# Kernel tuning notes

Hardware: AMD Instinct MI355X
Metric: run time of the kernel (lower is better)

## Reference

```python
import jax, jax.numpy as jnp
import numpy as np

N = 100000   # nodes
E = 800000   # directed edges (before self-loops)
D = 64       # hidden_dim
NUM_ROUNDS = 4
EPS = 1e-5


def setup_inputs() -> dict:
    key = jax.random.key(0)
    k0, k1, k2 = jax.random.split(key, 3)
    x = jax.random.normal(k0, (N, D), dtype=jnp.float32)
    edge_index = jax.random.randint(k1, (2, E), 0, N, dtype=jnp.int32)
    W = jax.random.normal(k2, (D, D), dtype=jnp.float32) * (1.0 / np.sqrt(D))
    b = jnp.zeros((D,), dtype=jnp.float32)
    gamma = jnp.ones((D,), dtype=jnp.float32)
    beta = jnp.zeros((D,), dtype=jnp.float32)
    return {"x": x, "edge_index": edge_index, "W": W, "b": b,
            "gamma": gamma, "beta": beta, "num_rounds": NUM_ROUNDS}


def reference(x, edge_index, W, b, gamma, beta, num_rounds):
    n = x.shape[0]
    # GCNConv: add self-loops, symmetric degree normalization D^-1/2 (A+I) D^-1/2
    loops = jnp.arange(n, dtype=edge_index.dtype)
    src = jnp.concatenate([edge_index[0], loops])  # [E+N] message sources
    dst = jnp.concatenate([edge_index[1], loops])  # [E+N] message targets
    deg = jax.ops.segment_sum(jnp.ones_like(dst, dtype=x.dtype), dst, num_segments=n)
    dis = jnp.where(deg > 0, jax.lax.rsqrt(deg), 0.0)  # deg^-1/2, 0 for isolated
    norm = dis[src] * dis[dst]                          # [E+N] edge weights

    for _ in range(num_rounds):
        h = x @ W                                                      # [N, D]
        msgs = h[src] * norm[:, None]                                  # gather [E+N, D]
        agg = jax.ops.segment_sum(msgs, dst, num_segments=n) + b      # scatter-add
        # LayerNorm over feature dim
        mu = agg.mean(axis=-1, keepdims=True)
        var = agg.var(axis=-1, keepdims=True)
        x = (agg - mu) * jax.lax.rsqrt(var + EPS) * gamma + beta
    return x
```

## Files before the change

### kernel.cpp

```cpp
#include <hip/hip_runtime.h>

#define D 64
#define EPSV 1e-5f
#define SLOTP 16
#define SLOTS2 24
#define BSH 9
#define BNODES (1 << BSH)
#define BCAP 8192
#define SRCBITS 17

typedef _Float16 f16;
typedef _Float16 f16x8 __attribute__((ext_vector_type(8)));
typedef float f32x4 __attribute__((ext_vector_type(4)));


__global__ void k_init(int* gcnt, int nbk, const float* __restrict__ W,
                       f16* __restrict__ Wp) {
    const int t = threadIdx.x;
    if (t < nbk) gcnt[t] = 0;
    for (int idx = t; idx < 512; idx += 256) {
        int s = idx >> 8, rem = idx & 255, tt = rem >> 6, l = rem & 63;
        int q = l >> 4, c = l & 15;
#pragma unroll
        for (int j = 0; j < 8; ++j) {
            int k = 32 * s + 8 * q + j;
            Wp[(size_t)idx * 8 + j] = (f16)W[k * D + 16 * tt + c];
        }
    }
}

__global__ __launch_bounds__(256) void k_binA(
    const int* __restrict__ src, const int* __restrict__ dst,
    int* __restrict__ gcnt, unsigned* __restrict__ breg, int e, int nbk) {
    __shared__ int bcnt[256];
    __shared__ int gbase[256];
    const int tid = threadIdx.x;
    if (tid < nbk) bcnt[tid] = 0;
    __syncthreads();

    const int per = (e + gridDim.x - 1) / gridDim.x;
    const int lo = blockIdx.x * per;
    const int hi = min(e, lo + per);

    for (int i = lo + tid; i < hi; i += 256)
        atomicAdd(&bcnt[dst[i] >> BSH], 1);
    __syncthreads();

    if (tid < nbk) {
        int c = bcnt[tid];
        gbase[tid] = (c > 0) ? atomicAdd(&gcnt[tid], c) : 0;
        bcnt[tid] = 0;
    }
    __syncthreads();

    for (int i = lo + tid; i < hi; i += 256) {
        int d_ = dst[i], s_ = src[i];
        int bkt = d_ >> BSH;
        int p = gbase[bkt] + atomicAdd(&bcnt[bkt], 1);
        if (p < BCAP)
            breg[(size_t)bkt * BCAP + p] =
                ((unsigned)(d_ & (BNODES - 1)) << SRCBITS) | (unsigned)s_;
    }
}

__global__ __launch_bounds__(256) void k_binB(
    const int* __restrict__ gcnt, const unsigned* __restrict__ breg,
    unsigned* __restrict__ slots, unsigned* __restrict__ slots2,
    int* __restrict__ cursor, float* __restrict__ disv, int n) {
    __shared__ int scnt[BNODES];
    __shared__ unsigned sbuf[BNODES][SLOTP];
    const int tid = threadIdx.x;
    const int bkt = blockIdx.x;
    const int base = bkt << BSH;
    const int nloc = min(BNODES, n - base);

    for (int i = tid; i < BNODES; i += 256) scnt[i] = 0;
    __syncthreads();

    const int cnt = min(gcnt[bkt], BCAP);
    const unsigned* reg = breg + (size_t)bkt * BCAP;
    for (int i = tid; i < cnt; i += 256) {
        unsigned v = reg[i];
        int ld = v >> SRCBITS;
        unsigned s = v & ((1u << SRCBITS) - 1);
        int p = atomicAdd(&scnt[ld], 1);
        if (p < SLOTP) sbuf[ld][p] = s;
        else if (p < SLOTP + SLOTS2)
            slots2[(size_t)(base + ld) * SLOTS2 + (p - SLOTP)] = s;
    }
    __syncthreads();

    for (int i = tid; i < nloc * 4; i += 256) {
        int ld = i >> 2, part = i & 3;
        ((uint4*)(slots + (size_t)(base + ld) * SLOTP))[part] =
            ((const uint4*)sbuf[ld])[part];
    }
    for (int i = tid; i < nloc; i += 256) {
        int c = scnt[i];
        cursor[base + i] = c;
        disv[base + i] = rsqrtf((float)(c + 1));
    }
}

__global__ __launch_bounds__(256) void k_xform(
    const float* __restrict__ x, const f16* __restrict__ Wp,
    const float* __restrict__ disv, f16* __restrict__ h, int n, int ntiles) {
    const int tile = blockIdx.x * 4 + (threadIdx.x >> 6);
    if (tile >= ntiles) return;
    const int lane = threadIdx.x & 63;
    const int q = lane >> 4, c = lane & 15;

    const f16x8* wp = (const f16x8*)Wp;
    f16x8 w0 = wp[0 * 64 + lane], w1 = wp[1 * 64 + lane];
    f16x8 w2 = wp[2 * 64 + lane], w3 = wp[3 * 64 + lane];
    f16x8 w4 = wp[4 * 64 + lane], w5 = wp[5 * 64 + lane];
    f16x8 w6 = wp[6 * 64 + lane], w7 = wp[7 * 64 + lane];

    const int row0 = tile * 16;
    const int rA = (row0 + c < n) ? (row0 + c) : (n - 1);

    const float4* xr = (const float4*)(x + (size_t)rA * D);
    float4 u0 = xr[2 * q], u1 = xr[2 * q + 1];
    float4 u2 = xr[8 + 2 * q], u3 = xr[9 + 2 * q];
    f16x8 a0 = (f16x8){(f16)u0.x, (f16)u0.y, (f16)u0.z, (f16)u0.w,
                       (f16)u1.x, (f16)u1.y, (f16)u1.z, (f16)u1.w};
    f16x8 a1 = (f16x8){(f16)u2.x, (f16)u2.y, (f16)u2.z, (f16)u2.w,
                       (f16)u3.x, (f16)u3.y, (f16)u3.z, (f16)u3.w};

    f32x4 d0 = {0,0,0,0}, d1 = {0,0,0,0}, d2 = {0,0,0,0}, d3 = {0,0,0,0};
    d0 = __builtin_amdgcn_mfma_f32_16x16x32_f16(a0, w0, d0, 0, 0, 0);
    d1 = __builtin_amdgcn_mfma_f32_16x16x32_f16(a0, w1, d1, 0, 0, 0);
    d2 = __builtin_amdgcn_mfma_f32_16x16x32_f16(a0, w2, d2, 0, 0, 0);
    d3 = __builtin_amdgcn_mfma_f32_16x16x32_f16(a0, w3, d3, 0, 0, 0);
    d0 = __builtin_amdgcn_mfma_f32_16x16x32_f16(a1, w4, d0, 0, 0, 0);
    d1 = __builtin_amdgcn_mfma_f32_16x16x32_f16(a1, w5, d1, 0, 0, 0);
    d2 = __builtin_amdgcn_mfma_f32_16x16x32_f16(a1, w6, d2, 0, 0, 0);
    d3 = __builtin_amdgcn_mfma_f32_16x16x32_f16(a1, w7, d3, 0, 0, 0);

    f32x4 dvv = *(const f32x4*)(disv + row0 + 4 * q);
#pragma unroll
    for (int r = 0; r < 4; ++r) {
        int row = row0 + q * 4 + r;
        if (row < n) {
            f16* hr = h + (size_t)row * D + c;
            hr[0]  = (f16)(d0[r] * dvv[r]);
            hr[16] = (f16)(d1[r] * dvv[r]);
            hr[32] = (f16)(d2[r] * dvv[r]);
            hr[48] = (f16)(d3[r] * dvv[r]);
        }
    }
}

template<bool LAST>
__global__ __launch_bounds__(256) void k_fuse(
    const f16* __restrict__ h, const unsigned* __restrict__ slots,
    const unsigned* __restrict__ slots2, const int* __restrict__ cursor,
    const float* __restrict__ disv,
    const float* __restrict__ bb, const float* __restrict__ gamma,
    const float* __restrict__ beta, const f16* __restrict__ Wp,
    float* __restrict__ out, f16* __restrict__ hnext, int n,
    int sq, int sr) {
    __shared__ __align__(16) f16 ylds[32][72];

    const int xb = blockIdx.x & 7, kb = blockIdx.x >> 3;
    const int bid = (xb < sr ? xb * (sq + 1) : sr * (sq + 1) + (xb - sr) * sq) + kb;

    const int tid = threadIdx.x;
    const int grp = tid >> 3;
    const int fl  = tid & 7;
    const int w = bid * 32 + grp;
    const bool act = (w < n);

    if (act) {
        const int jb = w * SLOTP;
        const int dg = cursor[w];
        const int dgp = (dg < SLOTP) ? dg : SLOTP;

        float acc[8];
        {
            f16x8 sv = *(const f16x8*)(h + (size_t)w * D + fl * 8);
#pragma unroll
            for (int f = 0; f < 8; ++f) acc[f] = (float)sv[f];
        }

        uint4 s0 = *(const uint4*)(slots + jb);
        uint4 s1 = *(const uint4*)(slots + jb + 4);
        uint4 s2 = *(const uint4*)(slots + jb + 8);
        const unsigned idx[12] = {s0.x, s0.y, s0.z, s0.w,
                                  s1.x, s1.y, s1.z, s1.w,
                                  s2.x, s2.y, s2.z, s2.w};
        f16x8 v[12];
#pragma unroll
        for (int k = 0; k < 12; ++k) {
            unsigned u = (k < dg) ? idx[k] : 0u;
            v[k] = *(const f16x8*)(h + (size_t)u * D + fl * 8);
        }
#pragma unroll
        for (int k = 0; k < 12; ++k) {
            float m = (k < dg) ? 1.0f : 0.0f;
#pragma unroll
            for (int f = 0; f < 8; ++f) acc[f] += m * (float)v[k][f];
        }
        if (dgp > 12) {
            uint4 sr4 = *(const uint4*)(slots + jb + 12);
            const unsigned uu[4] = {sr4.x, sr4.y, sr4.z, sr4.w};
#pragma unroll
            for (int k = 0; k < 4; ++k) {
                unsigned u = (12 + k < dgp) ? uu[k] : 0u;
                float m = (12 + k < dgp) ? 1.0f : 0.0f;
                f16x8 vv = *(const f16x8*)(h + (size_t)u * D + fl * 8);
#pragma unroll
                for (int f = 0; f < 8; ++f) acc[f] += m * (float)vv[f];
            }
        }
        if (dg > SLOTP) {
            const unsigned* r2 = slots2 + (size_t)w * SLOTS2;
            int dg2 = dg - SLOTP; if (dg2 > SLOTS2) dg2 = SLOTS2;
#pragma unroll
            for (int base = 0; base < SLOTS2; base += 4) {
                if (base < dg2) {
                    uint4 sr4 = *(const uint4*)(r2 + base);
                    const unsigned uu[4] = {sr4.x, sr4.y, sr4.z, sr4.w};
#pragma unroll
                    for (int k = 0; k < 4; ++k) {
                        unsigned u = (base + k < dg2) ? uu[k] : 0u;
                        float m = (base + k < dg2) ? 1.0f : 0.0f;
                        f16x8 vv = *(const f16x8*)(h + (size_t)u * D + fl * 8);
#pragma unroll
                        for (int f = 0; f < 8; ++f) acc[f] += m * (float)vv[f];
                    }
                }
            }
        }

        const float dv = disv[w];
        const float4 b0 = ((const float4*)bb)[fl * 2],    b1 = ((const float4*)bb)[fl * 2 + 1];
        const float4 g0 = ((const float4*)gamma)[fl * 2], g1 = ((const float4*)gamma)[fl * 2 + 1];
        const float4 e0 = ((const float4*)beta)[fl * 2],  e1 = ((const float4*)beta)[fl * 2 + 1];
        const float bs[8] = {b0.x, b0.y, b0.z, b0.w, b1.x, b1.y, b1.z, b1.w};
        const float gs[8] = {g0.x, g0.y, g0.z, g0.w, g1.x, g1.y, g1.z, g1.w};
        const float es[8] = {e0.x, e0.y, e0.z, e0.w, e1.x, e1.y, e1.z, e1.w};

#pragma unroll
        for (int f = 0; f < 8; ++f) acc[f] = acc[f] * dv + bs[f];

        float s = 0.0f;
#pragma unroll
        for (int f = 0; f < 8; ++f) s += acc[f];
#pragma unroll
        for (int m = 1; m < 8; m <<= 1) s += __shfl_xor(s, m);
        float mu = s * (1.0f / 64.0f);
        float dd[8], qv = 0.0f;
#pragma unroll
        for (int f = 0; f < 8; ++f) { dd[f] = acc[f] - mu; qv += dd[f] * dd[f]; }
#pragma unroll
        for (int m = 1; m < 8; m <<= 1) qv += __shfl_xor(qv, m);
        float rstd = rsqrtf(qv * (1.0f / 64.0f) + EPSV);

        if (LAST) {
            float4 o0, o1;
            o0.x = dd[0] * rstd * gs[0] + es[0]; o0.y = dd[1] * rstd * gs[1] + es[1];
            o0.z = dd[2] * rstd * gs[2] + es[2]; o0.w = dd[3] * rstd * gs[3] + es[3];
            o1.x = dd[4] * rstd * gs[4] + es[4]; o1.y = dd[5] * rstd * gs[5] + es[5];
            o1.z = dd[6] * rstd * gs[6] + es[6]; o1.w = dd[7] * rstd * gs[7] + es[7];
            float4* orow = (float4*)(out + (size_t)w * D);
            orow[fl * 2] = o0; orow[fl * 2 + 1] = o1;
        } else {
            f16x8 yv;
#pragma unroll
            for (int f = 0; f < 8; ++f) yv[f] = (f16)(dd[f] * rstd * gs[f] + es[f]);
            *(f16x8*)(&ylds[grp][fl * 8]) = yv;
        }
    }
    if (LAST) return;

    __syncthreads();

    const int wv = tid >> 6;
    const int lane = tid & 63;
    const int q = lane >> 4, c = lane & 15;

    const f16x8* wp = (const f16x8*)Wp;
    f16x8 wlo = wp[wv * 64 + lane];
    f16x8 whi = wp[(4 + wv) * 64 + lane];

    const int row0 = bid * 32;
#pragma unroll
    for (int rt = 0; rt < 2; ++rt) {
        f16x8 a0 = *(const f16x8*)(&ylds[rt * 16 + c][q * 8]);
        f16x8 a1 = *(const f16x8*)(&ylds[rt * 16 + c][32 + q * 8]);
        f32x4 d = {0, 0, 0, 0};
        d = __builtin_amdgcn_mfma_f32_16x16x32_f16(a0, wlo, d, 0, 0, 0);
        d = __builtin_amdgcn_mfma_f32_16x16x32_f16(a1, whi, d, 0, 0, 0);

        const int rbase = row0 + rt * 16;
        f32x4 dvv = *(const f32x4*)(disv + rbase + 4 * q);
#pragma unroll
        for (int r = 0; r < 4; ++r) {
            int row = rbase + q * 4 + r;
            if (row < n)
                hnext[(size_t)row * D + wv * 16 + c] = (f16)(d[r] * dvv[r]);
        }
    }
}


extern "C" void kernel_launch(void* const* d_in, const int* in_sizes, int n_in,
                              void* d_out, int out_size, void* d_ws, size_t ws_size,
                              hipStream_t stream) {
    const float* x0    = (const float*)d_in[0];
    const int*   ei    = (const int*)d_in[1];
    const float* W     = (const float*)d_in[2];
    const float* b     = (const float*)d_in[3];
    const float* gamma = (const float*)d_in[4];
    const float* beta  = (const float*)d_in[5];

    const int N = in_sizes[0] / D;
    const int E = in_sizes[1] / 2;
    const int* src = ei;
    const int* dst = ei + E;
    const int nbk = (N + BNODES - 1) >> BSH;

    char* ws = (char*)d_ws;
    size_t off = 0;
    auto alloc = [&](size_t bytes) {
        off = (off + 255) & ~(size_t)255;
        void* p = ws + off;
        off += bytes;
        return p;
    };
    int*      cursor = (int*)alloc((size_t)N * 4);
    unsigned* slots  = (unsigned*)alloc((size_t)N * SLOTP * 4);
    unsigned* slots2 = (unsigned*)alloc((size_t)N * SLOTS2 * 4);
    int*      gcnt   = (int*)alloc((size_t)nbk * 4);
    unsigned* breg   = (unsigned*)alloc((size_t)nbk * BCAP * 4);
    float*    disv   = (float*)alloc((size_t)(N + 32) * 4);
    f16*      Wp     = (f16*)alloc(512 * 8 * 2);
    f16*      hA     = (f16*)alloc((size_t)N * D * 2);
    f16*      hB     = (f16*)alloc((size_t)N * D * 2);
    (void)ws_size;

    k_init<<<1, 256, 0, stream>>>(gcnt, nbk, W, Wp);
    k_binA<<<128, 256, 0, stream>>>(src, dst, gcnt, breg, E, nbk);
    k_binB<<<nbk, 256, 0, stream>>>(gcnt, breg, slots, slots2, cursor, disv, N);

    float* out = (float*)d_out;
    const int ntiles = (N + 15) / 16;
    const int GX = (ntiles + 3) / 4;
    const int GG = (N + 31) / 32;
    const int sq = GG / 8, sr = GG % 8;

    k_xform<<<GX, 256, 0, stream>>>(x0, Wp, disv, hA, N, ntiles);
    k_fuse<false><<<GG, 256, 0, stream>>>(hA, slots, slots2, cursor, disv, b, gamma,
                                          beta, Wp, nullptr, hB, N, sq, sr);
    k_fuse<false><<<GG, 256, 0, stream>>>(hB, slots, slots2, cursor, disv, b, gamma,
                                          beta, Wp, nullptr, hA, N, sq, sr);
    k_fuse<false><<<GG, 256, 0, stream>>>(hA, slots, slots2, cursor, disv, b, gamma,
                                          beta, Wp, nullptr, hB, N, sq, sr);
    k_fuse<true><<<GG, 256, 0, stream>>>(hB, slots, slots2, cursor, disv, b, gamma,
                                         beta, Wp, out, nullptr, N, sq, sr);
}
```

Measured before the change: 215.2 us.

## Fuse input transform into binning kernel and pack degree into slot word

```diff
diff --git a/kernel.cpp b/kernel.cpp
--- a/kernel.cpp
+++ b/kernel.cpp
@@ -8,6 +8,8 @@
 #define BNODES (1 << BSH)
 #define BCAP 8192
 #define SRCBITS 17
+#define SRCMASK ((1u << SRCBITS) - 1)
+#define DGSHIFT 26
 
 typedef _Float16 f16;
 typedef _Float16 f16x8 __attribute__((ext_vector_type(8)));
@@ -66,7 +68,8 @@
 __global__ __launch_bounds__(256) void k_binB(
     const int* __restrict__ gcnt, const unsigned* __restrict__ breg,
     unsigned* __restrict__ slots, unsigned* __restrict__ slots2,
-    int* __restrict__ cursor, float* __restrict__ disv, int n) {
+    const float* __restrict__ x, const f16* __restrict__ Wp,
+    f16* __restrict__ h, int n) {
     __shared__ int scnt[BNODES];
     __shared__ unsigned sbuf[BNODES][SLOTP];
     const int tid = threadIdx.x;
@@ -74,7 +77,10 @@
     const int base = bkt << BSH;
     const int nloc = min(BNODES, n - base);
 
-    for (int i = tid; i < BNODES; i += 256) scnt[i] = 0;
+    for (int i = tid; i < BNODES; i += 256) {
+        scnt[i] = 0;
+        sbuf[i][0] = 0;
+    }
     __syncthreads();
 
     const int cnt = min(gcnt[bkt], BCAP);
@@ -82,7 +88,7 @@
     for (int i = tid; i < cnt; i += 256) {
         unsigned v = reg[i];
         int ld = v >> SRCBITS;
-        unsigned s = v & ((1u << SRCBITS) - 1);
+        unsigned s = v & SRCMASK;
         int p = atomicAdd(&scnt[ld], 1);
         if (p < SLOTP) sbuf[ld][p] = s;
         else if (p < SLOTP + SLOTS2)
@@ -92,75 +98,67 @@
 
     for (int i = tid; i < nloc * 4; i += 256) {
         int ld = i >> 2, part = i & 3;
-        ((uint4*)(slots + (size_t)(base + ld) * SLOTP))[part] =
-            ((const uint4*)sbuf[ld])[part];
-    }
-    for (int i = tid; i < nloc; i += 256) {
-        int c = scnt[i];
-        cursor[base + i] = c;
-        disv[base + i] = rsqrtf((float)(c + 1));
-    }
-}
-
-__global__ __launch_bounds__(256) void k_xform(
-    const float* __restrict__ x, const f16* __restrict__ Wp,
-    const float* __restrict__ disv, f16* __restrict__ h, int n, int ntiles) {
-    const int tile = blockIdx.x * 4 + (threadIdx.x >> 6);
-    if (tile >= ntiles) return;
-    const int lane = threadIdx.x & 63;
+        uint4 v = ((const uint4*)sbuf[ld])[part];
+        if (part == 0) v.x |= (unsigned)min(scnt[ld], 63) << DGSHIFT;
+        ((uint4*)(slots + (size_t)(base + ld) * SLOTP))[part] = v;
+    }
+
+    const int lane = tid & 63, wv = tid >> 6;
     const int q = lane >> 4, c = lane & 15;
-
     const f16x8* wp = (const f16x8*)Wp;
     f16x8 w0 = wp[0 * 64 + lane], w1 = wp[1 * 64 + lane];
     f16x8 w2 = wp[2 * 64 + lane], w3 = wp[3 * 64 + lane];
     f16x8 w4 = wp[4 * 64 + lane], w5 = wp[5 * 64 + lane];
     f16x8 w6 = wp[6 * 64 + lane], w7 = wp[7 * 64 + lane];
 
-    const int row0 = tile * 16;
-    const int rA = (row0 + c < n) ? (row0 + c) : (n - 1);
-
-    const float4* xr = (const float4*)(x + (size_t)rA * D);
-    float4 u0 = xr[2 * q], u1 = xr[2 * q + 1];
-    float4 u2 = xr[8 + 2 * q], u3 = xr[9 + 2 * q];
-    f16x8 a0 = (f16x8){(f16)u0.x, (f16)u0.y, (f16)u0.z, (f16)u0.w,
-                       (f16)u1.x, (f16)u1.y, (f16)u1.z, (f16)u1.w};
-    f16x8 a1 = (f16x8){(f16)u2.x, (f16)u2.y, (f16)u2.z, (f16)u2.w,
-                       (f16)u3.x, (f16)u3.y, (f16)u3.z, (f16)u3.w};
-
-    f32x4 d0 = {0,0,0,0}, d1 = {0,0,0,0}, d2 = {0,0,0,0}, d3 = {0,0,0,0};
-    d0 = __builtin_amdgcn_mfma_f32_16x16x32_f16(a0, w0, d0, 0, 0, 0);
-    d1 = __builtin_amdgcn_mfma_f32_16x16x32_f16(a0, w1, d1, 0, 0, 0);
-    d2 = __builtin_amdgcn_mfma_f32_16x16x32_f16(a0, w2, d2, 0, 0, 0);
-    d3 = __builtin_amdgcn_mfma_f32_16x16x32_f16(a0, w3, d3, 0, 0, 0);
-    d0 = __builtin_amdgcn_mfma_f32_16x16x32_f16(a1, w4, d0, 0, 0, 0);
-    d1 = __builtin_amdgcn_mfma_f32_16x16x32_f16(a1, w5, d1, 0, 0, 0);
-    d2 = __builtin_amdgcn_mfma_f32_16x16x32_f16(a1, w6, d2, 0, 0, 0);
-    d3 = __builtin_amdgcn_mfma_f32_16x16x32_f16(a1, w7, d3, 0, 0, 0);
-
-    f32x4 dvv = *(const f32x4*)(disv + row0 + 4 * q);
-#pragma unroll
-    for (int r = 0; r < 4; ++r) {
-        int row = row0 + q * 4 + r;
-        if (row < n) {
-            f16* hr = h + (size_t)row * D + c;
-            hr[0]  = (f16)(d0[r] * dvv[r]);
-            hr[16] = (f16)(d1[r] * dvv[r]);
-            hr[32] = (f16)(d2[r] * dvv[r]);
-            hr[48] = (f16)(d3[r] * dvv[r]);
+    for (int t = wv; t < 32; t += 4) {
+        const int row0 = base + t * 16;
+        if (row0 >= n) break;
+        const int rA = (row0 + c < n) ? (row0 + c) : (n - 1);
+
+        const float4* xr = (const float4*)(x + (size_t)rA * D);
+        float4 u0 = xr[2 * q], u1 = xr[2 * q + 1];
+        float4 u2 = xr[8 + 2 * q], u3 = xr[9 + 2 * q];
+        f16x8 a0 = (f16x8){(f16)u0.x, (f16)u0.y, (f16)u0.z, (f16)u0.w,
+                           (f16)u1.x, (f16)u1.y, (f16)u1.z, (f16)u1.w};
+        f16x8 a1 = (f16x8){(f16)u2.x, (f16)u2.y, (f16)u2.z, (f16)u2.w,
+                           (f16)u3.x, (f16)u3.y, (f16)u3.z, (f16)u3.w};
+
+        f32x4 d0 = {0,0,0,0}, d1 = {0,0,0,0}, d2 = {0,0,0,0}, d3 = {0,0,0,0};
+        d0 = __builtin_amdgcn_mfma_f32_16x16x32_f16(a0, w0, d0, 0, 0, 0);
+        d1 = __builtin_amdgcn_mfma_f32_16x16x32_f16(a0, w1, d1, 0, 0, 0);
+        d2 = __builtin_amdgcn_mfma_f32_16x16x32_f16(a0, w2, d2, 0, 0, 0);
+        d3 = __builtin_amdgcn_mfma_f32_16x16x32_f16(a0, w3, d3, 0, 0, 0);
+        d0 = __builtin_amdgcn_mfma_f32_16x16x32_f16(a1, w4, d0, 0, 0, 0);
+        d1 = __builtin_amdgcn_mfma_f32_16x16x32_f16(a1, w5, d1, 0, 0, 0);
+        d2 = __builtin_amdgcn_mfma_f32_16x16x32_f16(a1, w6, d2, 0, 0, 0);
+        d3 = __builtin_amdgcn_mfma_f32_16x16x32_f16(a1, w7, d3, 0, 0, 0);
+
+#pragma unroll
+        for (int r = 0; r < 4; ++r) {
+            int row = row0 + q * 4 + r;
+            if (row < n) {
+                float dvr = rsqrtf((float)(scnt[t * 16 + q * 4 + r] + 1));
+                f16* hr = h + (size_t)row * D + c;
+                hr[0]  = (f16)(d0[r] * dvr);
+                hr[16] = (f16)(d1[r] * dvr);
+                hr[32] = (f16)(d2[r] * dvr);
+                hr[48] = (f16)(d3[r] * dvr);
+            }
         }
     }
 }
 
 template<bool LAST>
-__global__ __launch_bounds__(256) void k_fuse(
+__global__ __launch_bounds__(256, 8) void k_fuse(
     const f16* __restrict__ h, const unsigned* __restrict__ slots,
-    const unsigned* __restrict__ slots2, const int* __restrict__ cursor,
-    const float* __restrict__ disv,
+    const unsigned* __restrict__ slots2,
     const float* __restrict__ bb, const float* __restrict__ gamma,
     const float* __restrict__ beta, const f16* __restrict__ Wp,
     float* __restrict__ out, f16* __restrict__ hnext, int n,
     int sq, int sr) {
     __shared__ __align__(16) f16 ylds[32][72];
+    __shared__ int dgs[32];
 
     const int xb = blockIdx.x & 7, kb = blockIdx.x >> 3;
     const int bid = (xb < sr ? xb * (sq + 1) : sr * (sq + 1) + (xb - sr) * sq) + kb;
@@ -173,8 +171,6 @@
 
     if (act) {
         const int jb = w * SLOTP;
-        const int dg = cursor[w];
-        const int dgp = (dg < SLOTP) ? dg : SLOTP;
 
         float acc[8];
         {
@@ -186,7 +182,9 @@
         uint4 s0 = *(const uint4*)(slots + jb);
         uint4 s1 = *(const uint4*)(slots + jb + 4);
         uint4 s2 = *(const uint4*)(slots + jb + 8);
-        const unsigned idx[12] = {s0.x, s0.y, s0.z, s0.w,
+        const int dg = (int)(s0.x >> DGSHIFT);
+        if (!LAST && fl == 0) dgs[grp] = dg;
+        const unsigned idx[12] = {s0.x & SRCMASK, s0.y, s0.z, s0.w,
                                   s1.x, s1.y, s1.z, s1.w,
                                   s2.x, s2.y, s2.z, s2.w};
         f16x8 v[12];
@@ -201,6 +199,7 @@
 #pragma unroll
             for (int f = 0; f < 8; ++f) acc[f] += m * (float)v[k][f];
         }
+        const int dgp = (dg < SLOTP) ? dg : SLOTP;
         if (dgp > 12) {
             uint4 sr4 = *(const uint4*)(slots + jb + 12);
             const unsigned uu[4] = {sr4.x, sr4.y, sr4.z, sr4.w};
@@ -233,7 +232,7 @@
             }
         }
 
-        const float dv = disv[w];
+        const float dv = rsqrtf((float)(dg + 1));
         const float4 b0 = ((const float4*)bb)[fl * 2],    b1 = ((const float4*)bb)[fl * 2 + 1];
         const float4 g0 = ((const float4*)gamma)[fl * 2], g1 = ((const float4*)gamma)[fl * 2 + 1];
         const float4 e0 = ((const float4*)beta)[fl * 2],  e1 = ((const float4*)beta)[fl * 2 + 1];
@@ -294,12 +293,13 @@
         d = __builtin_amdgcn_mfma_f32_16x16x32_f16(a1, whi, d, 0, 0, 0);
 
         const int rbase = row0 + rt * 16;
-        f32x4 dvv = *(const f32x4*)(disv + rbase + 4 * q);
 #pragma unroll
         for (int r = 0; r < 4; ++r) {
             int row = rbase + q * 4 + r;
-            if (row < n)
-                hnext[(size_t)row * D + wv * 16 + c] = (f16)(d[r] * dvv[r]);
+            if (row < n) {
+                float dvr = rsqrtf((float)(dgs[rt * 16 + q * 4 + r] + 1));
+                hnext[(size_t)row * D + wv * 16 + c] = (f16)(d[r] * dvr);
+            }
         }
     }
 }
@@ -329,12 +329,10 @@
         off += bytes;
         return p;
     };
-    int*      cursor = (int*)alloc((size_t)N * 4);
     unsigned* slots  = (unsigned*)alloc((size_t)N * SLOTP * 4);
     unsigned* slots2 = (unsigned*)alloc((size_t)N * SLOTS2 * 4);
     int*      gcnt   = (int*)alloc((size_t)nbk * 4);
     unsigned* breg   = (unsigned*)alloc((size_t)nbk * BCAP * 4);
-    float*    disv   = (float*)alloc((size_t)(N + 32) * 4);
     f16*      Wp     = (f16*)alloc(512 * 8 * 2);
     f16*      hA     = (f16*)alloc((size_t)N * D * 2);
     f16*      hB     = (f16*)alloc((size_t)N * D * 2);
@@ -342,21 +340,18 @@
 
     k_init<<<1, 256, 0, stream>>>(gcnt, nbk, W, Wp);
     k_binA<<<128, 256, 0, stream>>>(src, dst, gcnt, breg, E, nbk);
-    k_binB<<<nbk, 256, 0, stream>>>(gcnt, breg, slots, slots2, cursor, disv, N);
+    k_binB<<<nbk, 256, 0, stream>>>(gcnt, breg, slots, slots2, x0, Wp, hA, N);
 
     float* out = (float*)d_out;
-    const int ntiles = (N + 15) / 16;
-    const int GX = (ntiles + 3) / 4;
     const int GG = (N + 31) / 32;
     const int sq = GG / 8, sr = GG % 8;
 
-    k_xform<<<GX, 256, 0, stream>>>(x0, Wp, disv, hA, N, ntiles);
-    k_fuse<false><<<GG, 256, 0, stream>>>(hA, slots, slots2, cursor, disv, b, gamma,
-                                          beta, Wp, nullptr, hB, N, sq, sr);
-    k_fuse<false><<<GG, 256, 0, stream>>>(hB, slots, slots2, cursor, disv, b, gamma,
-                                          beta, Wp, nullptr, hA, N, sq, sr);
-    k_fuse<false><<<GG, 256, 0, stream>>>(hA, slots, slots2, cursor, disv, b, gamma,
-                                          beta, Wp, nullptr, hB, N, sq, sr);
-    k_fuse<true><<<GG, 256, 0, stream>>>(hB, slots, slots2, cursor, disv, b, gamma,
-                                         beta, Wp, out, nullptr, N, sq, sr);
-}
+    k_fuse<false><<<GG, 256, 0, stream>>>(hA, slots, slots2, b, gamma, beta,
+                                          Wp, nullptr, hB, N, sq, sr);
+    k_fuse<false><<<GG, 256, 0, stream>>>(hB, slots, slots2, b, gamma, beta,
+                                          Wp, nullptr, hA, N, sq, sr);
+    k_fuse<false><<<GG, 256, 0, stream>>>(hA, slots, slots2, b, gamma, beta,
+                                          Wp, nullptr, hB, N, sq, sr);
+    k_fuse<true><<<GG, 256, 0, stream>>>(hB, slots, slots2, b, gamma, beta,
+                                         Wp, out, nullptr, N, sq, sr);
+}
```

Result: slower. 248.3 us (+15.4%).
